# Optimization experiments

Measured on AMD Instinct MI355X. Metric: run time of the kernel, lower is better.

## Reference

```python
import jax, jax.numpy as jnp
import numpy as np

VOCAB, E, H = 53, 16, 32
B, S = 4096, 512


def setup_inputs() -> dict:
    key = jax.random.key(0)
    k = jax.random.split(key, 8)
    x = jax.random.randint(k[0], (B, S), 0, VOCAB)
    emb = jax.random.normal(k[1], (VOCAB, E), jnp.float32) * 0.1
    emb = emb.at[0].set(0.0)  # padding_idx=0 row is zero
    s = 1.0 / np.sqrt(H).astype(np.float32)
    W_ih = jax.random.uniform(k[2], (4 * H, E), jnp.float32, -s, s)
    W_hh = jax.random.uniform(k[3], (4 * H, H), jnp.float32, -s, s)
    b_ih = jax.random.uniform(k[4], (4 * H,), jnp.float32, -s, s)
    b_hh = jax.random.uniform(k[5], (4 * H,), jnp.float32, -s, s)
    sf = 1.0 / np.sqrt(H).astype(np.float32)
    W_fc = jax.random.uniform(k[6], (1, H), jnp.float32, -sf, sf)
    b_fc = jax.random.uniform(k[7], (1,), jnp.float32, -sf, sf)
    return {"x": x, "emb": emb, "W_ih": W_ih, "W_hh": W_hh,
            "b_ih": b_ih, "b_hh": b_hh, "W_fc": W_fc, "b_fc": b_fc}


def _lstm_last_hidden(ex, W_ih, W_hh, b_ih, b_hh):
    # ex: [B,S,E]. Precompute input contribution to all 4 gates: [B,S,4H]
    xg = jnp.einsum('bse,ge->bsg', ex, W_ih) + (b_ih + b_hh)
    b = ex.shape[0]
    h0 = jnp.zeros((b, H), ex.dtype)
    c0 = jnp.zeros((b, H), ex.dtype)

    def step(carry, xt):
        h, c = carry
        g = xt + h @ W_hh.T  # [B,4H]; torch gate order i,f,g,o
        i, f, gg, o = jnp.split(g, 4, axis=-1)
        c = jax.nn.sigmoid(f) * c + jax.nn.sigmoid(i) * jnp.tanh(gg)
        h = jax.nn.sigmoid(o) * jnp.tanh(c)
        return (h, c), None

    (hT, _), _ = jax.lax.scan(step, (h0, c0), jnp.swapaxes(xg, 0, 1))
    return hT  # [B,H]


def reference(x, emb, W_ih, W_hh, b_ih, b_hh, W_fc, b_fc):
    ex = emb[x]  # [B,S,E] embedding lookup
    hT = _lstm_last_hidden(ex, W_ih, W_hh, b_ih, b_hh)
    out = hT @ W_fc.T + b_fc  # [B,1]
    return jax.nn.sigmoid(out).squeeze()  # [B]
```

## Files before the change

kernel.cpp:

```cpp
#include <hip/hip_runtime.h>

#define VOCAB 53
#define EDIM  16
#define H     32
#define SEQ   512
#define BATCH 4096
#define LOG2E 1.4426950408889634f
#define XRS   132
#define HS    72
#define RSC   2048.0f
#define RSCI  (1.0f/2048.0f)

typedef _Float16 f16x8 __attribute__((ext_vector_type(8)));
typedef float f32x4 __attribute__((ext_vector_type(4)));

__device__ __forceinline__ float exp2_hw(float x) {
    float r; asm("v_exp_f32 %0, %1" : "=v"(r) : "v"(x)); return r;
}
__device__ __forceinline__ float sig_exp2(float xs) {
    return __builtin_amdgcn_rcpf(1.0f + exp2_hw(xs));
}

__device__ __forceinline__ void decode_row(int rp, int& orig, float& scale) {
    int m = rp >> 4, rem = rp & 15, s = rem >> 2, g = rem & 3;
    orig = g * 32 + 4 * m + s;
    scale = (g == 2) ? (-2.0f * LOG2E) : (-LOG2E);
}

__global__ __launch_bounds__(512, 1)
void lstm_seq_classifier(const int* __restrict__ x,
                         const float* __restrict__ emb,
                         const float* __restrict__ W_ih,
                         const float* __restrict__ W_hh,
                         const float* __restrict__ b_ih,
                         const float* __restrict__ b_hh,
                         const float* __restrict__ W_fc,
                         const float* __restrict__ b_fc,
                         float* __restrict__ out) {
    __shared__ float xg_perm[VOCAB * XRS];
    __shared__ _Float16 whi[128 * 32];
    __shared__ _Float16 wlo[128 * 32];
    __shared__ __align__(16) _Float16 hhi_buf[2][16][HS];
    __shared__ __align__(16) _Float16 hlo_buf[2][16][HS];
    __shared__ float red[16 * 33];

    const int tid  = threadIdx.x;
    const int lane = tid & 63;
    const int w    = tid >> 6;
    const int col  = lane & 15;
    const int q    = lane >> 4;

    for (int idx = tid; idx < VOCAB * 128; idx += 512) {
        int v = idx >> 7, rp = idx & 127;
        int orig; float scale; decode_row(rp, orig, scale);
        float acc = b_ih[orig] + b_hh[orig];
        const float* ev = emb + v * EDIM;
        const float* wr = W_ih + orig * EDIM;
#pragma unroll
        for (int e = 0; e < EDIM; ++e) acc += ev[e] * wr[e];
        xg_perm[v * XRS + rp] = scale * acc;
    }
    for (int idx = tid; idx < 128 * 32; idx += 512) {
        int rp = idx >> 5, k = idx & 31;
        int orig; float scale; decode_row(rp, orig, scale);
        float wv = scale * W_hh[orig * H + k];
        _Float16 hi = (_Float16)wv;
        whi[idx] = hi;
        wlo[idx] = (_Float16)((wv - (float)hi) * RSC);
    }
    for (int idx = tid; idx < 2 * 16 * HS; idx += 512) {
        (&hhi_buf[0][0][0])[idx] = (_Float16)0.f;
        (&hlo_buf[0][0][0])[idx] = (_Float16)0.f;
    }
    __syncthreads();

    const f16x8 Ahi = *reinterpret_cast<const f16x8*>(&whi[(16 * w + col) * 32 + 8 * q]);
    const f16x8 Alo = *reinterpret_cast<const f16x8*>(&wlo[(16 * w + col) * 32 + 8 * q]);

    const long xb = (long)(blockIdx.x * 16 + col) * SEQ;
    int vb = x[xb];
    int vc = x[xb + 1];
    f32x4 xg_cur = *reinterpret_cast<const f32x4*>(&xg_perm[vb * XRS + 16 * w + 4 * q]);

    float c = 0.0f, h = 0.0f;

    for (int s = 0; s < SEQ; ++s) {
        int vn = x[xb + ((s + 2) & (SEQ - 1))];
        f32x4 xg_nxt = *reinterpret_cast<const f32x4*>(
            &xg_perm[vc * XRS + 16 * w + 4 * q]);
        const int rb = s & 1;
        f16x8 Bhi = *reinterpret_cast<const f16x8*>(&hhi_buf[rb][col][8 * q]);
        f16x8 Blo = *reinterpret_cast<const f16x8*>(&hlo_buf[rb][col][8 * q]);

        f32x4 D  = __builtin_amdgcn_mfma_f32_16x16x32_f16(Ahi, Bhi, xg_cur, 0, 0, 0);
        f32x4 Dr = __builtin_amdgcn_mfma_f32_16x16x32_f16(Alo, Bhi,
                       f32x4{0.f, 0.f, 0.f, 0.f}, 0, 0, 0);
        Dr = __builtin_amdgcn_mfma_f32_16x16x32_f16(Ahi, Blo, Dr, 0, 0, 0);
        float zi = __builtin_fmaf(RSCI, Dr[0], D[0]);
        float zf = __builtin_fmaf(RSCI, Dr[1], D[1]);
        float zg = __builtin_fmaf(RSCI, Dr[2], D[2]);
        float zo = __builtin_fmaf(RSCI, Dr[3], D[3]);

        float si = sig_exp2(zi);
        float sf = sig_exp2(zf);
        float ug = sig_exp2(zg);
        float so = sig_exp2(zo);
        float gt = __builtin_fmaf(2.0f, ug, -1.0f);
        c = __builtin_fmaf(sf, c, si * gt);
        float tc = __builtin_fmaf(2.0f, sig_exp2(-2.0f * LOG2E * c), -1.0f);
        h = so * tc;

        const int nb = (s + 1) & 1;
        _Float16 hh = (_Float16)h;
        hhi_buf[nb][col][4 * w + q] = hh;
        hlo_buf[nb][col][4 * w + q] = (_Float16)((h - (float)hh) * RSC);
        __syncthreads();
        xg_cur = xg_nxt;
        vc = vn;
    }

    red[col * 33 + 4 * w + q] = h * W_fc[4 * w + q];
    __syncthreads();
    if (w == 0) {
        const float* rr = &red[col * 33];
        float p = 0.f;
#pragma unroll
        for (int u = 0; u < 8; ++u) p += rr[8 * q + u] ;
        p += __shfl_xor(p, 16);
        p += __shfl_xor(p, 32);
        if (lane < 16) {
            out[blockIdx.x * 16 + col] = sig_exp2(-LOG2E * (p + b_fc[0]));
        }
    }
}

extern "C" void kernel_launch(void* const* d_in, const int* in_sizes, int n_in,
                              void* d_out, int out_size, void* d_ws, size_t ws_size,
                              hipStream_t stream) {
    const int*   x    = (const int*)d_in[0];
    const float* emb  = (const float*)d_in[1];
    const float* W_ih = (const float*)d_in[2];
    const float* W_hh = (const float*)d_in[3];
    const float* b_ih = (const float*)d_in[4];
    const float* b_hh = (const float*)d_in[5];
    const float* W_fc = (const float*)d_in[6];
    const float* b_fc = (const float*)d_in[7];
    float* out = (float*)d_out;

    dim3 grid(BATCH / 16);
    dim3 block(512);
    lstm_seq_classifier<<<grid, block, 0, stream>>>(x, emb, W_ih, W_hh,
                                                    b_ih, b_hh, W_fc, b_fc, out);
}
```

Baseline: 159.4 us.

## Halve block to 4 waves with two gate tiles each, 8 sequences per block

After: 249.9 us. +56.8%, slower.

```diff
diff --git a/kernel.cpp b/kernel.cpp
--- a/kernel.cpp
+++ b/kernel.cpp
@@ -10,6 +10,7 @@
 #define HS    72
 #define RSC   2048.0f
 #define RSCI  (1.0f/2048.0f)
+#define CPB   8
 
 typedef _Float16 f16x8 __attribute__((ext_vector_type(8)));
 typedef float f32x4 __attribute__((ext_vector_type(4)));
@@ -27,7 +28,7 @@
     scale = (g == 2) ? (-2.0f * LOG2E) : (-LOG2E);
 }
 
-__global__ __launch_bounds__(512, 1)
+__global__ __launch_bounds__(256, 2)
 void lstm_seq_classifier(const int* __restrict__ x,
                          const float* __restrict__ emb,
                          const float* __restrict__ W_ih,
@@ -50,7 +51,7 @@
     const int col  = lane & 15;
     const int q    = lane >> 4;
 
-    for (int idx = tid; idx < VOCAB * 128; idx += 512) {
+    for (int idx = tid; idx < VOCAB * 128; idx += 256) {
         int v = idx >> 7, rp = idx & 127;
         int orig; float scale; decode_row(rp, orig, scale);
         float acc = b_ih[orig] + b_hh[orig];
@@ -60,7 +61,7 @@
         for (int e = 0; e < EDIM; ++e) acc += ev[e] * wr[e];
         xg_perm[v * XRS + rp] = scale * acc;
     }
-    for (int idx = tid; idx < 128 * 32; idx += 512) {
+    for (int idx = tid; idx < 128 * 32; idx += 256) {
         int rp = idx >> 5, k = idx & 31;
         int orig; float scale; decode_row(rp, orig, scale);
         float wv = scale * W_hh[orig * H + k];
@@ -68,68 +69,96 @@
         whi[idx] = hi;
         wlo[idx] = (_Float16)((wv - (float)hi) * RSC);
     }
-    for (int idx = tid; idx < 2 * 16 * HS; idx += 512) {
+    for (int idx = tid; idx < 2 * 16 * HS; idx += 256) {
         (&hhi_buf[0][0][0])[idx] = (_Float16)0.f;
         (&hlo_buf[0][0][0])[idx] = (_Float16)0.f;
     }
     __syncthreads();
 
-    const f16x8 Ahi = *reinterpret_cast<const f16x8*>(&whi[(16 * w + col) * 32 + 8 * q]);
-    const f16x8 Alo = *reinterpret_cast<const f16x8*>(&wlo[(16 * w + col) * 32 + 8 * q]);
+    const int c0 = 2 * w, c1 = 2 * w + 1;
+    const f16x8 Ahi0 = *reinterpret_cast<const f16x8*>(&whi[(16 * c0 + col) * 32 + 8 * q]);
+    const f16x8 Alo0 = *reinterpret_cast<const f16x8*>(&wlo[(16 * c0 + col) * 32 + 8 * q]);
+    const f16x8 Ahi1 = *reinterpret_cast<const f16x8*>(&whi[(16 * c1 + col) * 32 + 8 * q]);
+    const f16x8 Alo1 = *reinterpret_cast<const f16x8*>(&wlo[(16 * c1 + col) * 32 + 8 * q]);
 
-    const long xb = (long)(blockIdx.x * 16 + col) * SEQ;
+    int elem = blockIdx.x * CPB + col;
+    if (elem > BATCH - 1) elem = BATCH - 1;
+    const long xb = (long)elem * SEQ;
     int vb = x[xb];
     int vc = x[xb + 1];
-    f32x4 xg_cur = *reinterpret_cast<const f32x4*>(&xg_perm[vb * XRS + 16 * w + 4 * q]);
+    f32x4 xg_cur0 = *reinterpret_cast<const f32x4*>(&xg_perm[vb * XRS + 16 * c0 + 4 * q]);
+    f32x4 xg_cur1 = *reinterpret_cast<const f32x4*>(&xg_perm[vb * XRS + 16 * c1 + 4 * q]);
 
-    float c = 0.0f, h = 0.0f;
+    float cc0 = 0.0f, hh0 = 0.0f;
+    float cc1 = 0.0f, hh1 = 0.0f;
 
     for (int s = 0; s < SEQ; ++s) {
         int vn = x[xb + ((s + 2) & (SEQ - 1))];
-        f32x4 xg_nxt = *reinterpret_cast<const f32x4*>(
-            &xg_perm[vc * XRS + 16 * w + 4 * q]);
+        f32x4 xg_nxt0 = *reinterpret_cast<const f32x4*>(
+            &xg_perm[vc * XRS + 16 * c0 + 4 * q]);
+        f32x4 xg_nxt1 = *reinterpret_cast<const f32x4*>(
+            &xg_perm[vc * XRS + 16 * c1 + 4 * q]);
         const int rb = s & 1;
         f16x8 Bhi = *reinterpret_cast<const f16x8*>(&hhi_buf[rb][col][8 * q]);
         f16x8 Blo = *reinterpret_cast<const f16x8*>(&hlo_buf[rb][col][8 * q]);
 
-        f32x4 D  = __builtin_amdgcn_mfma_f32_16x16x32_f16(Ahi, Bhi, xg_cur, 0, 0, 0);
-        f32x4 Dr = __builtin_amdgcn_mfma_f32_16x16x32_f16(Alo, Bhi,
-                       f32x4{0.f, 0.f, 0.f, 0.f}, 0, 0, 0);
-        Dr = __builtin_amdgcn_mfma_f32_16x16x32_f16(Ahi, Blo, Dr, 0, 0, 0);
-        float zi = __builtin_fmaf(RSCI, Dr[0], D[0]);
-        float zf = __builtin_fmaf(RSCI, Dr[1], D[1]);
-        float zg = __builtin_fmaf(RSCI, Dr[2], D[2]);
-        float zo = __builtin_fmaf(RSCI, Dr[3], D[3]);
+        f32x4 D0  = __builtin_amdgcn_mfma_f32_16x16x32_f16(Ahi0, Bhi, xg_cur0, 0, 0, 0);
+        f32x4 Dr0 = __builtin_amdgcn_mfma_f32_16x16x32_f16(Alo0, Bhi,
+                        f32x4{0.f, 0.f, 0.f, 0.f}, 0, 0, 0);
+        Dr0 = __builtin_amdgcn_mfma_f32_16x16x32_f16(Ahi0, Blo, Dr0, 0, 0, 0);
+        f32x4 D1  = __builtin_amdgcn_mfma_f32_16x16x32_f16(Ahi1, Bhi, xg_cur1, 0, 0, 0);
+        f32x4 Dr1 = __builtin_amdgcn_mfma_f32_16x16x32_f16(Alo1, Bhi,
+                        f32x4{0.f, 0.f, 0.f, 0.f}, 0, 0, 0);
+        Dr1 = __builtin_amdgcn_mfma_f32_16x16x32_f16(Ahi1, Blo, Dr1, 0, 0, 0);
 
-        float si = sig_exp2(zi);
-        float sf = sig_exp2(zf);
-        float ug = sig_exp2(zg);
-        float so = sig_exp2(zo);
-        float gt = __builtin_fmaf(2.0f, ug, -1.0f);
-        c = __builtin_fmaf(sf, c, si * gt);
-        float tc = __builtin_fmaf(2.0f, sig_exp2(-2.0f * LOG2E * c), -1.0f);
-        h = so * tc;
+        {
+            float zi = __builtin_fmaf(RSCI, Dr0[0], D0[0]);
+            float zf = __builtin_fmaf(RSCI, Dr0[1], D0[1]);
+            float zg = __builtin_fmaf(RSCI, Dr0[2], D0[2]);
+            float zo = __builtin_fmaf(RSCI, Dr0[3], D0[3]);
+            float si = sig_exp2(zi), sf = sig_exp2(zf);
+            float ug = sig_exp2(zg), so = sig_exp2(zo);
+            float gt = __builtin_fmaf(2.0f, ug, -1.0f);
+            cc0 = __builtin_fmaf(sf, cc0, si * gt);
+            float tc = __builtin_fmaf(2.0f, sig_exp2(-2.0f * LOG2E * cc0), -1.0f);
+            hh0 = so * tc;
+        }
+        {
+            float zi = __builtin_fmaf(RSCI, Dr1[0], D1[0]);
+            float zf = __builtin_fmaf(RSCI, Dr1[1], D1[1]);
+            float zg = __builtin_fmaf(RSCI, Dr1[2], D1[2]);
+            float zo = __builtin_fmaf(RSCI, Dr1[3], D1[3]);
+            float si = sig_exp2(zi), sf = sig_exp2(zf);
+            float ug = sig_exp2(zg), so = sig_exp2(zo);
+            float gt = __builtin_fmaf(2.0f, ug, -1.0f);
+            cc1 = __builtin_fmaf(sf, cc1, si * gt);
+            float tc = __builtin_fmaf(2.0f, sig_exp2(-2.0f * LOG2E * cc1), -1.0f);
+            hh1 = so * tc;
+        }
 
         const int nb = (s + 1) & 1;
-        _Float16 hh = (_Float16)h;
-        hhi_buf[nb][col][4 * w + q] = hh;
-        hlo_buf[nb][col][4 * w + q] = (_Float16)((h - (float)hh) * RSC);
+        _Float16 h0h = (_Float16)hh0, h1h = (_Float16)hh1;
+        hhi_buf[nb][col][8 * w + q]     = h0h;
+        hhi_buf[nb][col][8 * w + 4 + q] = h1h;
+        hlo_buf[nb][col][8 * w + q]     = (_Float16)((hh0 - (float)h0h) * RSC);
+        hlo_buf[nb][col][8 * w + 4 + q] = (_Float16)((hh1 - (float)h1h) * RSC);
         __syncthreads();
-        xg_cur = xg_nxt;
+        xg_cur0 = xg_nxt0; xg_cur1 = xg_nxt1;
         vc = vn;
     }
 
-    red[col * 33 + 4 * w + q] = h * W_fc[4 * w + q];
+    red[col * 33 + 8 * w + q]     = hh0 * W_fc[8 * w + q];
+    red[col * 33 + 8 * w + 4 + q] = hh1 * W_fc[8 * w + 4 + q];
     __syncthreads();
     if (w == 0) {
         const float* rr = &red[col * 33];
         float p = 0.f;
 #pragma unroll
-        for (int u = 0; u < 8; ++u) p += rr[8 * q + u] ;
+        for (int u = 0; u < 8; ++u) p += rr[8 * q + u];
         p += __shfl_xor(p, 16);
         p += __shfl_xor(p, 32);
-        if (lane < 16) {
-            out[blockIdx.x * 16 + col] = sig_exp2(-LOG2E * (p + b_fc[0]));
+        if (lane < CPB) {
+            out[blockIdx.x * CPB + lane] = sig_exp2(-LOG2E * (p + b_fc[0]));
         }
     }
 }
@@ -147,8 +176,8 @@
     const float* b_fc = (const float*)d_in[7];
     float* out = (float*)d_out;
 
-    dim3 grid(BATCH / 16);
-    dim3 block(512);
+    dim3 grid(BATCH / CPB);
+    dim3 block(256);
     lstm_seq_classifier<<<grid, block, 0, stream>>>(x, emb, W_ih, W_hh,
                                                     b_ih, b_hh, W_fc, b_fc, out);
 }
```

## Pack hi/lo hidden halves into one shared word and decouple residual MFMAs

Applied to the files above, without the earlier changes.

Measured after the change: 226.5 us. 42.1% more time.

```diff
diff --git a/kernel.cpp b/kernel.cpp
--- a/kernel.cpp
+++ b/kernel.cpp
@@ -7,7 +7,7 @@
 #define BATCH 4096
 #define LOG2E 1.4426950408889634f
 #define XRS   132
-#define HS    72
+#define HUS   36
 #define RSC   2048.0f
 #define RSCI  (1.0f/2048.0f)
 
@@ -40,8 +40,7 @@
     __shared__ float xg_perm[VOCAB * XRS];
     __shared__ _Float16 whi[128 * 32];
     __shared__ _Float16 wlo[128 * 32];
-    __shared__ __align__(16) _Float16 hhi_buf[2][16][HS];
-    __shared__ __align__(16) _Float16 hlo_buf[2][16][HS];
+    __shared__ __align__(16) unsigned hb[2][16][HUS];
     __shared__ float red[16 * 33];
 
     const int tid  = threadIdx.x;
@@ -68,53 +67,71 @@
         whi[idx] = hi;
         wlo[idx] = (_Float16)((wv - (float)hi) * RSC);
     }
-    for (int idx = tid; idx < 2 * 16 * HS; idx += 512) {
-        (&hhi_buf[0][0][0])[idx] = (_Float16)0.f;
-        (&hlo_buf[0][0][0])[idx] = (_Float16)0.f;
-    }
+    for (int idx = tid; idx < 2 * 16 * HUS; idx += 512)
+        (&hb[0][0][0])[idx] = 0u;
     __syncthreads();
 
     const f16x8 Ahi = *reinterpret_cast<const f16x8*>(&whi[(16 * w + col) * 32 + 8 * q]);
     const f16x8 Alo = *reinterpret_cast<const f16x8*>(&wlo[(16 * w + col) * 32 + 8 * q]);
 
     const long xb = (long)(blockIdx.x * 16 + col) * SEQ;
-    int vb = x[xb];
     int vc = x[xb + 1];
-    f32x4 xg_cur = *reinterpret_cast<const f32x4*>(&xg_perm[vb * XRS + 16 * w + 4 * q]);
+    f32x4 xg_cur = *reinterpret_cast<const f32x4*>(&xg_perm[x[xb] * XRS + 16 * w + 4 * q]);
 
-    float c = 0.0f, h = 0.0f;
+    const unsigned* rd  = &hb[0][col][8 * q];
+    const unsigned* rdN = &hb[1][col][8 * q];
+    unsigned* wr_  = &hb[1][col][4 * w + q];
+    unsigned* wrN  = &hb[0][col][4 * w + q];
+
+    float ccs = 0.0f, h = 0.0f;
+
+    const f32x4 zeroC = {0.f, 0.f, 0.f, 0.f};
 
     for (int s = 0; s < SEQ; ++s) {
         int vn = x[xb + ((s + 2) & (SEQ - 1))];
         f32x4 xg_nxt = *reinterpret_cast<const f32x4*>(
             &xg_perm[vc * XRS + 16 * w + 4 * q]);
-        const int rb = s & 1;
-        f16x8 Bhi = *reinterpret_cast<const f16x8*>(&hhi_buf[rb][col][8 * q]);
-        f16x8 Blo = *reinterpret_cast<const f16x8*>(&hlo_buf[rb][col][8 * q]);
 
-        f32x4 D  = __builtin_amdgcn_mfma_f32_16x16x32_f16(Ahi, Bhi, xg_cur, 0, 0, 0);
-        f32x4 Dr = __builtin_amdgcn_mfma_f32_16x16x32_f16(Alo, Bhi,
-                       f32x4{0.f, 0.f, 0.f, 0.f}, 0, 0, 0);
-        Dr = __builtin_amdgcn_mfma_f32_16x16x32_f16(Ahi, Blo, Dr, 0, 0, 0);
-        float zi = __builtin_fmaf(RSCI, Dr[0], D[0]);
-        float zf = __builtin_fmaf(RSCI, Dr[1], D[1]);
-        float zg = __builtin_fmaf(RSCI, Dr[2], D[2]);
-        float zo = __builtin_fmaf(RSCI, Dr[3], D[3]);
+        uint4 u0 = *reinterpret_cast<const uint4*>(rd);
+        uint4 u1 = *reinterpret_cast<const uint4*>(rd + 4);
+        union { unsigned u[4]; f16x8 v; } bh, bl;
+        bh.u[0] = (u0.x & 0xFFFFu) | (u0.y << 16);
+        bh.u[1] = (u0.z & 0xFFFFu) | (u0.w << 16);
+        bh.u[2] = (u1.x & 0xFFFFu) | (u1.y << 16);
+        bh.u[3] = (u1.z & 0xFFFFu) | (u1.w << 16);
+        bl.u[0] = (u0.x >> 16) | (u0.y & 0xFFFF0000u);
+        bl.u[1] = (u0.z >> 16) | (u0.w & 0xFFFF0000u);
+        bl.u[2] = (u1.x >> 16) | (u1.y & 0xFFFF0000u);
+        bl.u[3] = (u1.z >> 16) | (u1.w & 0xFFFF0000u);
+
+        f32x4 D   = __builtin_amdgcn_mfma_f32_16x16x32_f16(Ahi, bh.v, xg_cur, 0, 0, 0);
+        f32x4 Dra = __builtin_amdgcn_mfma_f32_16x16x32_f16(Alo, bh.v, zeroC, 0, 0, 0);
+        f32x4 Drb = __builtin_amdgcn_mfma_f32_16x16x32_f16(Ahi, bl.v, zeroC, 0, 0, 0);
+
+        float zi = __builtin_fmaf(RSCI, Dra[0] + Drb[0], D[0]);
+        float zf = __builtin_fmaf(RSCI, Dra[1] + Drb[1], D[1]);
+        float zg = __builtin_fmaf(RSCI, Dra[2] + Drb[2], D[2]);
+        float zo = __builtin_fmaf(RSCI, Dra[3] + Drb[3], D[3]);
 
         float si = sig_exp2(zi);
         float sf = sig_exp2(zf);
         float ug = sig_exp2(zg);
         float so = sig_exp2(zo);
-        float gt = __builtin_fmaf(2.0f, ug, -1.0f);
-        c = __builtin_fmaf(sf, c, si * gt);
-        float tc = __builtin_fmaf(2.0f, sig_exp2(-2.0f * LOG2E * c), -1.0f);
+        float t1 = __builtin_fmaf(-4.0f * LOG2E, ug, 2.0f * LOG2E);
+        ccs = __builtin_fmaf(sf, ccs, si * t1);
+        float tc = __builtin_fmaf(2.0f, sig_exp2(ccs), -1.0f);
         h = so * tc;
 
-        const int nb = (s + 1) & 1;
-        _Float16 hh = (_Float16)h;
-        hhi_buf[nb][col][4 * w + q] = hh;
-        hlo_buf[nb][col][4 * w + q] = (_Float16)((h - (float)hh) * RSC);
+        _Float16 hf = (_Float16)h;
+        float lof = (h - (float)hf) * RSC;
+        _Float16 lf = (_Float16)lof;
+        unsigned pw = (unsigned)__builtin_bit_cast(unsigned short, hf)
+                    | ((unsigned)__builtin_bit_cast(unsigned short, lf) << 16);
+        wr_[0] = pw;
         __syncthreads();
+
+        { const unsigned* t = rd; rd = rdN; rdN = t; }
+        { unsigned* t = wr_; wr_ = wrN; wrN = t; }
         xg_cur = xg_nxt;
         vc = vn;
     }
@@ -125,7 +142,7 @@
         const float* rr = &red[col * 33];
         float p = 0.f;
 #pragma unroll
-        for (int u = 0; u < 8; ++u) p += rr[8 * q + u] ;
+        for (int u = 0; u < 8; ++u) p += rr[8 * q + u];
         p += __shfl_xor(p, 16);
         p += __shfl_xor(p, 32);
         if (lane < 16) {
```

## Move vocab gate table to a global prepass kernel and shorten recurrence chain

Applied to the files above, without the earlier changes.

Measured after the change: 232.2 us. +45.7%, slower.

```diff
diff --git a/kernel.cpp b/kernel.cpp
--- a/kernel.cpp
+++ b/kernel.cpp
@@ -6,7 +6,6 @@
 #define SEQ   512
 #define BATCH 4096
 #define LOG2E 1.4426950408889634f
-#define XRS   132
 #define HS    72
 #define RSC   2048.0f
 #define RSCI  (1.0f/2048.0f)
@@ -27,17 +26,30 @@
     scale = (g == 2) ? (-2.0f * LOG2E) : (-LOG2E);
 }
 
+__global__ void build_xg(const float* __restrict__ emb,
+                         const float* __restrict__ W_ih,
+                         const float* __restrict__ b_ih,
+                         const float* __restrict__ b_hh,
+                         float* __restrict__ xg_g) {
+    int idx = blockIdx.x * 256 + threadIdx.x;
+    if (idx >= VOCAB * 128) return;
+    int v = idx >> 7, rp = idx & 127;
+    int orig; float scale; decode_row(rp, orig, scale);
+    float acc = b_ih[orig] + b_hh[orig];
+    const float* ev = emb + v * EDIM;
+    const float* wr = W_ih + orig * EDIM;
+#pragma unroll
+    for (int e = 0; e < EDIM; ++e) acc += ev[e] * wr[e];
+    xg_g[v * 128 + rp] = scale * acc;
+}
+
 __global__ __launch_bounds__(512, 1)
 void lstm_seq_classifier(const int* __restrict__ x,
-                         const float* __restrict__ emb,
-                         const float* __restrict__ W_ih,
                          const float* __restrict__ W_hh,
-                         const float* __restrict__ b_ih,
-                         const float* __restrict__ b_hh,
                          const float* __restrict__ W_fc,
                          const float* __restrict__ b_fc,
+                         const float* __restrict__ xg_g,
                          float* __restrict__ out) {
-    __shared__ float xg_perm[VOCAB * XRS];
     __shared__ _Float16 whi[128 * 32];
     __shared__ _Float16 wlo[128 * 32];
     __shared__ __align__(16) _Float16 hhi_buf[2][16][HS];
@@ -50,16 +62,6 @@
     const int col  = lane & 15;
     const int q    = lane >> 4;
 
-    for (int idx = tid; idx < VOCAB * 128; idx += 512) {
-        int v = idx >> 7, rp = idx & 127;
-        int orig; float scale; decode_row(rp, orig, scale);
-        float acc = b_ih[orig] + b_hh[orig];
-        const float* ev = emb + v * EDIM;
-        const float* wr = W_ih + orig * EDIM;
-#pragma unroll
-        for (int e = 0; e < EDIM; ++e) acc += ev[e] * wr[e];
-        xg_perm[v * XRS + rp] = scale * acc;
-    }
     for (int idx = tid; idx < 128 * 32; idx += 512) {
         int rp = idx >> 5, k = idx & 31;
         int orig; float scale; decode_row(rp, orig, scale);
@@ -78,42 +80,42 @@
     const f16x8 Alo = *reinterpret_cast<const f16x8*>(&wlo[(16 * w + col) * 32 + 8 * q]);
 
     const long xb = (long)(blockIdx.x * 16 + col) * SEQ;
-    int vb = x[xb];
+    const int xoff = 16 * w + 4 * q;
     int vc = x[xb + 1];
-    f32x4 xg_cur = *reinterpret_cast<const f32x4*>(&xg_perm[vb * XRS + 16 * w + 4 * q]);
+    f32x4 xg_cur = *reinterpret_cast<const f32x4*>(&xg_g[x[xb] * 128 + xoff]);
 
-    float c = 0.0f, h = 0.0f;
+    float ccs = 0.0f, h = 0.0f;
+    const f32x4 zeroC = {0.f, 0.f, 0.f, 0.f};
 
     for (int s = 0; s < SEQ; ++s) {
         int vn = x[xb + ((s + 2) & (SEQ - 1))];
         f32x4 xg_nxt = *reinterpret_cast<const f32x4*>(
-            &xg_perm[vc * XRS + 16 * w + 4 * q]);
-        const int rb = s & 1;
+            &xg_g[vc * 128 + xoff]);
+        const int rb = s & 1, nb = s & 1 ? 0 : 1;
         f16x8 Bhi = *reinterpret_cast<const f16x8*>(&hhi_buf[rb][col][8 * q]);
         f16x8 Blo = *reinterpret_cast<const f16x8*>(&hlo_buf[rb][col][8 * q]);
 
-        f32x4 D  = __builtin_amdgcn_mfma_f32_16x16x32_f16(Ahi, Bhi, xg_cur, 0, 0, 0);
-        f32x4 Dr = __builtin_amdgcn_mfma_f32_16x16x32_f16(Alo, Bhi,
-                       f32x4{0.f, 0.f, 0.f, 0.f}, 0, 0, 0);
-        Dr = __builtin_amdgcn_mfma_f32_16x16x32_f16(Ahi, Blo, Dr, 0, 0, 0);
-        float zi = __builtin_fmaf(RSCI, Dr[0], D[0]);
-        float zf = __builtin_fmaf(RSCI, Dr[1], D[1]);
-        float zg = __builtin_fmaf(RSCI, Dr[2], D[2]);
-        float zo = __builtin_fmaf(RSCI, Dr[3], D[3]);
+        f32x4 D   = __builtin_amdgcn_mfma_f32_16x16x32_f16(Ahi, Bhi, xg_cur, 0, 0, 0);
+        f32x4 Dra = __builtin_amdgcn_mfma_f32_16x16x32_f16(Alo, Bhi, zeroC, 0, 0, 0);
+        f32x4 Drb = __builtin_amdgcn_mfma_f32_16x16x32_f16(Ahi, Blo, zeroC, 0, 0, 0);
+
+        float zi = __builtin_fmaf(RSCI, Dra[0] + Drb[0], D[0]);
+        float zf = __builtin_fmaf(RSCI, Dra[1] + Drb[1], D[1]);
+        float zg = __builtin_fmaf(RSCI, Dra[2] + Drb[2], D[2]);
+        float zo = __builtin_fmaf(RSCI, Dra[3] + Drb[3], D[3]);
 
         float si = sig_exp2(zi);
         float sf = sig_exp2(zf);
         float ug = sig_exp2(zg);
         float so = sig_exp2(zo);
-        float gt = __builtin_fmaf(2.0f, ug, -1.0f);
-        c = __builtin_fmaf(sf, c, si * gt);
-        float tc = __builtin_fmaf(2.0f, sig_exp2(-2.0f * LOG2E * c), -1.0f);
+        float t1 = __builtin_fmaf(-4.0f * LOG2E, ug, 2.0f * LOG2E);
+        ccs = __builtin_fmaf(sf, ccs, si * t1);
+        float tc = __builtin_fmaf(2.0f, sig_exp2(ccs), -1.0f);
         h = so * tc;
 
-        const int nb = (s + 1) & 1;
-        _Float16 hh = (_Float16)h;
-        hhi_buf[nb][col][4 * w + q] = hh;
-        hlo_buf[nb][col][4 * w + q] = (_Float16)((h - (float)hh) * RSC);
+        _Float16 hf = (_Float16)h;
+        hhi_buf[nb][col][4 * w + q] = hf;
+        hlo_buf[nb][col][4 * w + q] = (_Float16)((h - (float)hf) * RSC);
         __syncthreads();
         xg_cur = xg_nxt;
         vc = vn;
@@ -125,7 +127,7 @@
         const float* rr = &red[col * 33];
         float p = 0.f;
 #pragma unroll
-        for (int u = 0; u < 8; ++u) p += rr[8 * q + u] ;
+        for (int u = 0; u < 8; ++u) p += rr[8 * q + u];
         p += __shfl_xor(p, 16);
         p += __shfl_xor(p, 32);
         if (lane < 16) {
@@ -145,10 +147,14 @@
     const float* b_hh = (const float*)d_in[5];
     const float* W_fc = (const float*)d_in[6];
     const float* b_fc = (const float*)d_in[7];
-    float* out = (float*)d_out;
+    float* out  = (float*)d_out;
+    float* xg_g = (float*)d_ws;
+
+    dim3 gb((VOCAB * 128 + 255) / 256);
+    build_xg<<<gb, 256, 0, stream>>>(emb, W_ih, b_ih, b_hh, xg_g);
 
     dim3 grid(BATCH / 16);
     dim3 block(512);
-    lstm_seq_classifier<<<grid, block, 0, stream>>>(x, emb, W_ih, W_hh,
-                                                    b_ih, b_hh, W_fc, b_fc, out);
+    lstm_seq_classifier<<<grid, block, 0, stream>>>(x, W_hh, W_fc, b_fc,
+                                                    xg_g, out);
 }
```
